# Performance work log

Measured on AMD Instinct MI355X. Metric: run time of the kernel, lower is better.

Reference implementation:

```python
import jax, jax.numpy as jnp
import numpy as np

N, IN, HID, OUT, HD = 512, 256, 256, 256, 64  # n_agents, in_dim, hid_dim, out_dim, head_dim (out_dim // n_heads)


def _mlp2(x, w1, b1, w2, b2):
    return jax.nn.relu(x @ w1.T + b1) @ w2.T + b2


def setup_inputs():
    key = jax.random.key(0)
    ks = jax.random.split(key, 32)
    p = lambda i, shape: jax.random.normal(ks[i], shape, dtype=jnp.float32) * 0.05
    V = jax.random.normal(ks[0], (N, IN), dtype=jnp.float32)
    adj = jax.random.randint(ks[1], (N, N), 0, 2, dtype=jnp.int32)
    adj = adj.at[jnp.arange(N), jnp.arange(N)].set(1)  # self-loops so no softmax row is all -inf
    prev_hidden = jax.random.normal(ks[2], (N, HID), dtype=jnp.float32)
    return {
        "V": V, "adj": adj, "prev_hidden": prev_hidden,
        "W1": p(3, (HID, IN)), "sa0": p(4, (HID,)), "sa1": p(5, (HID,)),
        "ce_w1": p(6, (HID, 2 * IN)), "ce_b1": p(7, (HID,)), "ce_w2": p(8, (HD, HID)), "ce_b2": p(9, (HD,)),
        "ca0": p(10, (HD,)), "ca1": p(11, (HD,)),
        "te_w1": p(12, (HID, IN + HID)), "te_b1": p(13, (HID,)), "te_w2": p(14, (HD, HID)), "te_b2": p(15, (HD,)),
        "ta0": p(16, (HD,)), "ta1": p(17, (HD,)),
        "pe_w1": p(18, (HID, 3 * IN)), "pe_b1": p(19, (HID,)), "pe_w2": p(20, (HD, HID)), "pe_b2": p(21, (HD,)),
        "pa0": p(22, (HD,)), "pa1": p(23, (HD,)),
        "W2": p(24, (OUT, HID + 2 * HD + 1)), "op_w": p(25, (OUT, OUT)), "op_b": p(26, (OUT,)),
        "ln_g": jnp.ones((OUT,), jnp.float32), "ln_b": jnp.zeros((OUT,), jnp.float32),
    }


def _forward(V, adj, prev_hidden, W1, sa0, sa1, ce_w1, ce_b1, ce_w2, ce_b2, ca0, ca1,
             te_w1, te_b1, te_w2, te_b2, ta0, ta1, pe_w1, pe_b1, pe_w2, pe_b2, pa0, pa1,
             W2, op_w, op_b, ln_g, ln_b):
    neg = -jnp.inf
    # --- branch 1: standard GAT attention ---
    Wh1 = V @ W1.T                                             # (N, HID)
    s1 = (Wh1 @ sa0)[:, None] + (Wh1 @ sa1)[None, :]           # (N, N)
    s1 = jnp.where(adj == 0, neg, s1)
    H1 = jax.nn.softmax(s1, axis=1) @ Wh1                      # (N, HID)
    # --- branch 2: causal, all ordered pairs i != j ---
    wA, wB = ce_w1[:, :IN], ce_w1[:, IN:]
    h = jax.nn.relu((V @ wA.T)[:, None, :] + (V @ wB.T)[None, :, :] + ce_b1)  # (N, N, HID)
    f = h @ ce_w2.T + ce_b2                                    # (N, N, HD)
    s2 = jnp.where(jnp.eye(N, dtype=bool), neg, f @ (ca0 + ca1))
    a2 = jax.nn.softmax(s2.reshape(-1)).reshape(N, N)          # softmax over all off-diagonal pairs
    H2 = jnp.broadcast_to(jnp.einsum('ij,ijd->d', a2, f), (N, HD))
    # --- branch 3: temporal; (N,1) scores broadcast against (N,N) causal mask ---
    tf = _mlp2(jnp.concatenate([V, prev_hidden], -1), te_w1, te_b1, te_w2, te_b2)  # (N, HD)
    ts = tf @ (ta0 + ta1)                                      # (N,)
    cmask = jnp.triu(jnp.ones((N, N), dtype=bool), 1)
    s3 = jnp.where(cmask, neg, jnp.broadcast_to(ts[:, None], (N, N)))
    H3 = jax.nn.softmax(s3, axis=1) @ tf                       # (N, HD) == prefix means of tf
    # --- branch 4: cooperative; first two neighbors in index order (zeros if < 2) ---
    pos = jnp.where(adj == 1, jnp.arange(N)[None, :], N)
    srt = jnp.sort(pos, axis=1)
    i0, i1 = srt[:, 0], srt[:, 1]
    valid = (i1 < N)[:, None]
    n0 = jnp.where(valid, V[jnp.clip(i0, 0, N - 1)], 0.0)
    n1 = jnp.where(valid, V[jnp.clip(i1, 0, N - 1)], 0.0)
    cf = _mlp2(jnp.concatenate([V, n0, n1], -1), pe_w1, pe_b1, pe_w2, pe_b2)  # (N, HD)
    # torch: softmax over dim of size 1 -> all ones, alpha^T @ cf == column sums -> (HD,)
    # then unsqueezed to (HD,1) and zero-padded to (N,1) since HD < N  (faithful to source bug)
    H4v = cf.sum(axis=0)
    H4 = jnp.concatenate([H4v, jnp.zeros((N - HD,), V.dtype)])[:, None]       # (N, 1)
    # --- combine ---
    Hc = jnp.concatenate([H1, H2, H3, H4], axis=-1) @ W2.T     # (N, OUT)
    out = Hc @ op_w.T + op_b
    mu = out.mean(-1, keepdims=True)
    var = ((out - mu) ** 2).mean(-1, keepdims=True)
    y = (out - mu) / jnp.sqrt(var + 1e-5) * ln_g + ln_b        # LayerNorm, eps=1e-5
    return jax.nn.elu(y)                                       # dropout is identity in eval


def reference(V, adj, prev_hidden, W1, sa0, sa1, ce_w1, ce_b1, ce_w2, ce_b2, ca0, ca1,
              te_w1, te_b1, te_w2, te_b2, ta0, ta1, pe_w1, pe_b1, pe_w2, pe_b2, pa0, pa1,
              W2, op_w, op_b, ln_g, ln_b):
    return _forward(V, adj, prev_hidden, W1, sa0, sa1, ce_w1, ce_b1, ce_w2, ce_b2, ca0, ca1,
                    te_w1, te_b1, te_w2, te_b2, ta0, ta1, pe_w1, pe_b1, pe_w2, pe_b2, pa0, pa1,
                    W2, op_w, op_b, ln_g, ln_b)
```

## Files before the change

kernel.cpp:

```cpp
#include <hip/hip_runtime.h>

typedef unsigned short u16;

constexpr int kN   = 512;
constexpr int kIN  = 256;
constexpr int kHID = 256;
constexpr int kHD  = 64;
constexpr int kOUT = 256;

__device__ __forceinline__ float us2f(u16 u){
  union { unsigned int i; float f; } c; c.i = ((unsigned int)u) << 16; return c.f;
}
__device__ __forceinline__ u16 f2us(float f){
  union { float f; unsigned int i; } c; c.f = f;
  unsigned int r = c.i + 0x7fff + ((c.i >> 16) & 1);
  return (u16)(r >> 16);
}

__global__ void k_probe(const unsigned int* __restrict__ V, int* __restrict__ flag){
  __shared__ int cnt;
  if (threadIdx.x == 0) cnt = 0;
  __syncthreads();
  int c = 0;
  for (int k = threadIdx.x; k < 4096; k += 256){
    float x = us2f((u16)(V[k] & 0xffffu));
    float ax = fabsf(x);
    if (!(ax <= 32.0f)) c++;
  }
  atomicAdd(&cnt, c);
  __syncthreads();
  if (threadIdx.x == 0) *flag = (cnt > 64) ? 1 : 0;
}

struct ConvArgs { const void* src[23]; float* dst[23]; int n[23]; };

__global__ void k_convert_all(ConvArgs a, const int* __restrict__ flag){
  bool f32 = (*flag != 0);
  int stride = gridDim.x * blockDim.x;
  int t = blockIdx.x * blockDim.x + threadIdx.x;
  for (int s = 0; s < 23; ++s){
    int n4 = a.n[s] >> 2;
    float4* d = (float4*)a.dst[s];
    if (f32){
      const float4* sf = (const float4*)a.src[s];
      for (int i = t; i < n4; i += stride) d[i] = sf[i];
    } else {
      const ushort4* sb = (const ushort4*)a.src[s];
      for (int i = t; i < n4; i += stride){
        ushort4 u = sb[i];
        d[i] = make_float4(us2f(u.x), us2f(u.y), us2f(u.z), us2f(u.w));
      }
    }
  }
}

__device__ __forceinline__ float blk_red(float v, float* tmp, bool isMax){
  int lane = threadIdx.x & 63, wv = threadIdx.x >> 6;
  #pragma unroll
  for (int o = 32; o > 0; o >>= 1){
    float t = __shfl_down(v, o, 64);
    v = isMax ? fmaxf(v, t) : (v + t);
  }
  __syncthreads();
  if (lane == 0) tmp[wv] = v;
  __syncthreads();
  float r = tmp[0];
  for (int i = 1; i < 4; ++i) r = isMax ? fmaxf(r, tmp[i]) : (r + tmp[i]);
  return r;
}

struct WSP {
  const int* adj; const int* flag; void* out;
  float *Vf,*prevf,*W1f,*sa1f,*cw1f,*cb1f,*cw2f,*cb2f,*ca0f,*ca1f;
  float *tw1f,*tb1f,*tw2f,*tb2f,*pw1f,*pb1f,*pw2f,*pb2f;
  float *W2f,*opwf,*opbf,*lngf,*lnbf;
  float *Wh1,*e1v,*minv,*invzv,*H1p,*H1,*Am,*Bm,*uvec,*beta;
  float *s2,*maxp,*zp,*MZ,*gsum,*c2v;
  float *htp0,*htp1,*hpp0,*hpp1,*hpp2,*hidden_t,*hidden_p;
  float *tfp0,*tfp1,*tfp2,*tfp3,*cfp0,*cfp1,*cfp2,*cfp3;
  float *tfm,*cfm,*H3,*H4v,*Xp;
};

struct GSeg2 { const float* X; const float* W; float* C; int ldx, ldw, ldc, K; };
struct GArgs2 { GSeg2 s[8]; };

__device__ __forceinline__ void gemm_body(const GSeg2 sg, int tm, int tn, int tid,
                                          float* xsB, float* wsB)
{
  const int i0 = tm << 7;
  const int n0 = tn << 6;
  const int xrow = tid >> 3;
  const int xk   = (tid & 7) << 2;
  const int rg = (tid >> 4) << 3;
  const int cg = (tid & 15) << 2;

  const float* Xb = sg.X + (size_t)i0 * sg.ldx;
  const float* Wb = sg.W + (size_t)n0 * sg.ldw;

  float4 xr[4], wr[2];
  auto loadT = [&](int kt){
    #pragma unroll
    for (int i2 = 0; i2 < 4; ++i2)
      xr[i2] = *(const float4*)(Xb + (size_t)(xrow + 32*i2) * sg.ldx + kt + xk);
    #pragma unroll
    for (int i2 = 0; i2 < 2; ++i2)
      wr[i2] = *(const float4*)(Wb + (size_t)(xrow + 32*i2) * sg.ldw + kt + xk);
  };
  auto writeT = [&](int bu){
    float* xs = xsB + bu*4224;
    #pragma unroll
    for (int i2 = 0; i2 < 4; ++i2){
      xs[(xk+0)*132 + xrow+32*i2] = xr[i2].x;
      xs[(xk+1)*132 + xrow+32*i2] = xr[i2].y;
      xs[(xk+2)*132 + xrow+32*i2] = xr[i2].z;
      xs[(xk+3)*132 + xrow+32*i2] = xr[i2].w;
    }
    float* ws2 = wsB + bu*2176;
    #pragma unroll
    for (int i2 = 0; i2 < 2; ++i2){
      ws2[(xk+0)*68 + xrow+32*i2] = wr[i2].x;
      ws2[(xk+1)*68 + xrow+32*i2] = wr[i2].y;
      ws2[(xk+2)*68 + xrow+32*i2] = wr[i2].z;
      ws2[(xk+3)*68 + xrow+32*i2] = wr[i2].w;
    }
  };

  loadT(0); writeT(0); __syncthreads();

  float acc[8][4] = {};
  const int nkt = sg.K >> 5;
  for (int t = 0; t < nkt; ++t){
    if (t + 1 < nkt) loadT((t + 1) << 5);
    const float* xs  = xsB + (t & 1)*4224;
    const float* ws2 = wsB + (t & 1)*2176;
    #pragma unroll
    for (int kk = 0; kk < 32; ++kk){
      const float4 a0 = *(const float4*)&xs[kk*132 + rg];
      const float4 a1 = *(const float4*)&xs[kk*132 + rg + 4];
      const float4 bv = *(const float4*)&ws2[kk*68 + cg];
      acc[0][0]+=a0.x*bv.x; acc[0][1]+=a0.x*bv.y; acc[0][2]+=a0.x*bv.z; acc[0][3]+=a0.x*bv.w;
      acc[1][0]+=a0.y*bv.x; acc[1][1]+=a0.y*bv.y; acc[1][2]+=a0.y*bv.z; acc[1][3]+=a0.y*bv.w;
      acc[2][0]+=a0.z*bv.x; acc[2][1]+=a0.z*bv.y; acc[2][2]+=a0.z*bv.z; acc[2][3]+=a0.z*bv.w;
      acc[3][0]+=a0.w*bv.x; acc[3][1]+=a0.w*bv.y; acc[3][2]+=a0.w*bv.z; acc[3][3]+=a0.w*bv.w;
      acc[4][0]+=a1.x*bv.x; acc[4][1]+=a1.x*bv.y; acc[4][2]+=a1.x*bv.z; acc[4][3]+=a1.x*bv.w;
      acc[5][0]+=a1.y*bv.x; acc[5][1]+=a1.y*bv.y; acc[5][2]+=a1.y*bv.z; acc[5][3]+=a1.y*bv.w;
      acc[6][0]+=a1.z*bv.x; acc[6][1]+=a1.z*bv.y; acc[6][2]+=a1.z*bv.z; acc[6][3]+=a1.z*bv.w;
      acc[7][0]+=a1.w*bv.x; acc[7][1]+=a1.w*bv.y; acc[7][2]+=a1.w*bv.z; acc[7][3]+=a1.w*bv.w;
    }
    if (t + 1 < nkt) writeT((t + 1) & 1);
    __syncthreads();
  }

  #pragma unroll
  for (int ri = 0; ri < 8; ++ri)
    *(float4*)(sg.C + (size_t)(i0 + rg + ri) * sg.ldc + (n0 + cg)) =
      make_float4(acc[ri][0], acc[ri][1], acc[ri][2], acc[ri][3]);
}

__global__ __launch_bounds__(256) void k_gemmA(GArgs2 ga)
{
  __shared__ __align__(16) float xsB[2*4224];
  __shared__ __align__(16) float wsB[2*2176];
  const GSeg2 sg = ga.s[blockIdx.y];
  gemm_body(sg, blockIdx.x & 3, blockIdx.x >> 2, threadIdx.x, xsB, wsB);
}

__global__ __launch_bounds__(256) void k_packsel(const int* __restrict__ adj,
                                                 const float* __restrict__ Vf,
                                                 float* __restrict__ Xp)
{
  __shared__ unsigned long long msk[8];
  __shared__ int sj[2];
  int i = blockIdx.x, tid = threadIdx.x;
  int w = tid >> 6, lane = tid & 63;
  unsigned long long m0 = __ballot(adj[(size_t)i*kN + tid] != 0);
  unsigned long long m1 = __ballot(adj[(size_t)i*kN + 256 + tid] != 0);
  if (lane == 0){ msk[w] = m0; msk[4 + w] = m1; }
  __syncthreads();
  if (tid == 0){
    int j0 = -1, j1 = -1;
    for (int c = 0; c < 8 && j1 < 0; ++c){
      unsigned long long m = msk[c];
      while (m && j1 < 0){
        int b = __builtin_ctzll(m);
        int j = c*64 + b;
        if (j0 < 0) j0 = j; else j1 = j;
        m &= m - 1;
      }
    }
    if (j1 < 0) j0 = -1;
    sj[0] = j0; sj[1] = j1;
  }
  __syncthreads();
  int j0 = sj[0], j1 = sj[1];
  Xp[(size_t)i*768 + tid]       = Vf[(size_t)i*kIN + tid];
  Xp[(size_t)i*768 + 256 + tid] = (j0 >= 0) ? Vf[(size_t)j0*kIN + tid] : 0.f;
  Xp[(size_t)i*768 + 512 + tid] = (j1 >= 0) ? Vf[(size_t)j1*kIN + tid] : 0.f;
}

__global__ __launch_bounds__(256) void k_stage2(WSP w)
{
  __shared__ float sm[64];
  int b = blockIdx.x, tid = threadIdx.x;
  if (b < 128){
    int f = b*256 + tid;
    int c4 = f & 63;
    {
      float4 a = ((const float4*)w.htp0)[f], bb = ((const float4*)w.htp1)[f];
      float4 bi = ((const float4*)w.tb1f)[c4];
      ((float4*)w.hidden_t)[f] = make_float4(
        fmaxf(a.x+bb.x+bi.x,0.f), fmaxf(a.y+bb.y+bi.y,0.f),
        fmaxf(a.z+bb.z+bi.z,0.f), fmaxf(a.w+bb.w+bi.w,0.f));
    }
    {
      float4 a = ((const float4*)w.hpp0)[f], bb = ((const float4*)w.hpp1)[f];
      float4 c = ((const float4*)w.hpp2)[f];
      float4 bi = ((const float4*)w.pb1f)[c4];
      ((float4*)w.hidden_p)[f] = make_float4(
        fmaxf(a.x+bb.x+c.x+bi.x,0.f), fmaxf(a.y+bb.y+c.y+bi.y,0.f),
        fmaxf(a.z+bb.z+c.z+bi.z,0.f), fmaxf(a.w+bb.w+c.w+bi.w,0.f));
    }
  } else if (b < 256){
    int r = (b-128)*4 + (tid >> 6), lane = tid & 63;
    float a = 0.f;
    for (int k = lane; k < kHID; k += 64) a += w.Wh1[(size_t)r*kHID + k] * w.sa1f[k];
    #pragma unroll
    for (int o = 32; o > 0; o >>= 1) a += __shfl_down(a, o, 64);
    if (lane == 0) w.e1v[r] = a;
  } else {
    if (tid < 64){ sm[tid] = w.ca0f[tid] + w.ca1f[tid]; w.H4v[tid] = 0.f; }
    __syncthreads();
    float a = 0.f;
    for (int d = 0; d < kHD; ++d) a += w.cw2f[(size_t)d*kHID + tid] * sm[d];
    w.uvec[tid] = a;
    if (tid == 0){
      float bsum = 0.f;
      for (int d = 0; d < kHD; ++d) bsum += w.cb2f[d] * sm[d];
      *w.beta = bsum;
    }
  }
}

__global__ __launch_bounds__(256) void k_stage3(WSP w, GArgs2 gb)
{
  __shared__ __align__(16) char smem[51200];
  int b = blockIdx.x, tid = threadIdx.x;
  if (b < 32){
    const GSeg2 sg = gb.s[b >> 2];
    gemm_body(sg, b & 3, 0, tid, (float*)smem, (float*)(smem + 33792));
  } else if (b < 544){
    float* red = (float*)smem;
    int i = b - 32;
    int m0 = w.adj[(size_t)i*kN + tid];
    int m1 = w.adj[(size_t)i*kN + tid + 256];
    float ea = w.e1v[tid], eb = w.e1v[tid+256];
    float v0 = m0 ? ea : -1e30f;
    float v1 = m1 ? eb : -1e30f;
    float m = blk_red(fmaxf(v0, v1), red, true);
    float z = blk_red((m0 ? expf(ea-m) : 0.f) + (m1 ? expf(eb-m) : 0.f), red, false);
    if (tid == 0){ w.minv[i] = m; w.invzv[i] = 1.0f / z; }
  } else {
    float* aib = (float*)smem;
    float* uu  = (float*)(smem + 4096);
    int q = b - 544;
    int i0 = (q & 127) * 4, j0 = (q >> 7) * 64;
    int wv = tid >> 6, lane = tid & 63;
    uu[tid] = w.uvec[tid];
    float b1v = w.cb1f[tid];
    #pragma unroll
    for (int r = 0; r < 4; ++r) aib[r*256 + tid] = w.Am[(size_t)(i0+r)*kHID + tid] + b1v;
    __syncthreads();
    int i = i0 + wv, j = j0 + lane;
    const float4* bp = (const float4*)(w.Bm + (size_t)j*kHID);
    float acc = *w.beta;
    #pragma unroll 8
    for (int k4 = 0; k4 < kHID/4; ++k4){
      float4 bv = bp[k4];
      float4 a4 = *(const float4*)&aib[wv*256 + k4*4];
      float4 u4 = *(const float4*)&uu[k4*4];
      acc += fmaxf(a4.x+bv.x,0.f)*u4.x + fmaxf(a4.y+bv.y,0.f)*u4.y
           + fmaxf(a4.z+bv.z,0.f)*u4.z + fmaxf(a4.w+bv.w,0.f)*u4.w;
    }
    if (j == i) acc = -1e30f;
    w.s2[(size_t)i*kN + j] = acc;
    float m = acc;
    #pragma unroll
    for (int o = 32; o > 0; o >>= 1) m = fmaxf(m, __shfl_down(m, o, 64));
    m = __shfl(m, 0, 64);
    float e = expf(acc - m);
    #pragma unroll
    for (int o = 32; o > 0; o >>= 1) e += __shfl_down(e, o, 64);
    if (lane == 0){
      int pb = q*4 + wv;
      w.maxp[pb] = m; w.zp[pb] = e;
    }
  }
}

__global__ __launch_bounds__(256) void k_stage4(WSP w)
{
  __shared__ __align__(16) char smem[4096];
  int b = blockIdx.x, tid = threadIdx.x;
  if (b < 32){
    int f = b*256 + tid;
    int c4 = f & 15;
    {
      float4 a = ((const float4*)w.tfp0)[f], bb = ((const float4*)w.tfp1)[f];
      float4 c = ((const float4*)w.tfp2)[f], d = ((const float4*)w.tfp3)[f];
      float4 bi = ((const float4*)w.tb2f)[c4];
      ((float4*)w.tfm)[f] = make_float4(a.x+bb.x+c.x+d.x+bi.x, a.y+bb.y+c.y+d.y+bi.y,
                                        a.z+bb.z+c.z+d.z+bi.z, a.w+bb.w+c.w+d.w+bi.w);
    }
    float4 cc;
    {
      float4 a = ((const float4*)w.cfp0)[f], bb = ((const float4*)w.cfp1)[f];
      float4 c = ((const float4*)w.cfp2)[f], d = ((const float4*)w.cfp3)[f];
      float4 bi = ((const float4*)w.pb2f)[c4];
      cc = make_float4(a.x+bb.x+c.x+d.x+bi.x, a.y+bb.y+c.y+d.y+bi.y,
                       a.z+bb.z+c.z+d.z+bi.z, a.w+bb.w+c.w+d.w+bi.w);
      ((float4*)w.cfm)[f] = cc;
    }
    float4* red4 = (float4*)smem;
    red4[tid] = cc;
    __syncthreads();
    #pragma unroll
    for (int st = 128; st >= 16; st >>= 1){
      if (tid < st){
        float4 x = red4[tid], y = red4[tid + st];
        red4[tid] = make_float4(x.x+y.x, x.y+y.y, x.z+y.z, x.w+y.w);
      }
      __syncthreads();
    }
    if (tid < 16){
      float4 v = red4[tid];
      atomicAdd(&w.H4v[tid*4+0], v.x);
      atomicAdd(&w.H4v[tid*4+1], v.y);
      atomicAdd(&w.H4v[tid*4+2], v.z);
      atomicAdd(&w.H4v[tid*4+3], v.w);
    }
  } else if (b < 1056){
    float* wt = (float*)smem;
    int q = b - 32;
    int i0 = (q & 127) * 4, jt = q >> 7, j0 = jt * 64;
    {
      int r = tid >> 6, jj = tid & 63;
      int j = j0 + jj;
      wt[r*64 + jj] = w.adj[(size_t)(i0+r)*kN + j]
                    ? expf(w.e1v[j] - w.minv[i0+r]) * w.invzv[i0+r] : 0.f;
    }
    __syncthreads();
    float a0=0,a1=0,a2=0,a3=0;
    #pragma unroll 4
    for (int jj = 0; jj < 64; ++jj){
      float wh = w.Wh1[(size_t)(j0+jj)*kHID + tid];
      a0 += wt[jj]*wh; a1 += wt[64+jj]*wh; a2 += wt[128+jj]*wh; a3 += wt[192+jj]*wh;
    }
    size_t base = ((size_t)jt*kN + i0)*kHID + tid;
    w.H1p[base]          = a0;
    w.H1p[base + kHID]   = a1;
    w.H1p[base + 2*kHID] = a2;
    w.H1p[base + 3*kHID] = a3;
  } else {
    float* red = (float*)smem;
    float m = -1e30f;
    #pragma unroll
    for (int r = 0; r < 16; ++r) m = fmaxf(m, w.maxp[tid + 256*r]);
    m = blk_red(m, red, true);
    float z = 0.f;
    #pragma unroll
    for (int r = 0; r < 16; ++r) z += w.zp[tid + 256*r] * expf(w.maxp[tid + 256*r] - m);
    z = blk_red(z, red, false);
    if (tid == 0){ w.MZ[0] = m; w.MZ[1] = z; }
    w.gsum[tid] = 0.f;
  }
}

__global__ __launch_bounds__(256) void k_stage5(WSP w)
{
  __shared__ __align__(16) char smem[1536];
  int b = blockIdx.x, tid = threadIdx.x;
  if (b < 1024){
    float* wt = (float*)smem;
    int i0 = (b & 31) * 16, j0 = (b >> 5) * 16;
    float M = w.MZ[0], invZ = 1.0f / w.MZ[1];
    {
      int r = tid >> 4, c = tid & 15;
      wt[r*16 + c] = expf(w.s2[(size_t)(i0+r)*kN + (j0+c)] - M) * invZ;
    }
    float b1v = w.cb1f[tid];
    float aib[16];
    #pragma unroll
    for (int r = 0; r < 16; ++r) aib[r] = w.Am[(size_t)(i0+r)*kHID + tid] + b1v;
    __syncthreads();
    float acc = 0.f;
    for (int j = 0; j < 16; ++j){
      float bj = w.Bm[(size_t)(j0+j)*kHID + tid];
      #pragma unroll
      for (int r = 0; r < 16; ++r)
        acc += wt[r*16 + j] * fmaxf(aib[r] + bj, 0.f);
    }
    atomicAdd(&w.gsum[tid], acc);
  } else if (b < 1536){
    int i = b - 1024;
    float s = 0.f;
    #pragma unroll
    for (int jt = 0; jt < 8; ++jt)
      s += w.H1p[((size_t)jt*kN + i)*kHID + tid];
    w.H1[(size_t)i*kHID + tid] = s;
  } else {
    int d = b - 1536;
    int lane = tid & 63, wv = tid >> 6;
    float v0 = w.tfm[(size_t)(2*tid)*kHD + d];
    float v1 = w.tfm[(size_t)(2*tid+1)*kHD + d];
    float s = v0 + v1;
    float x = s;
    #pragma unroll
    for (int off = 1; off < 64; off <<= 1){
      float y = __shfl_up(x, off, 64);
      if (lane >= off) x += y;
    }
    float* wsum = (float*)smem;
    if (lane == 63) wsum[wv] = x;
    __syncthreads();
    float base = 0.f;
    for (int k = 0; k < wv; ++k) base += wsum[k];
    float excl = base + x - s;
    w.H3[(size_t)(2*tid)*kHD + d]   = (excl + v0) / (float)(2*tid + 1);
    w.H3[(size_t)(2*tid+1)*kHD + d] = (excl + s)  / (float)(2*tid + 2);
  }
}

__global__ void k_h2c(WSP w)
{
  __shared__ float gs[kHID];
  __shared__ float part[kHD][4];
  __shared__ float h2s[kHD];
  int tid = threadIdx.x;
  gs[tid] = w.gsum[tid];
  __syncthreads();
  int d = tid >> 2, q = tid & 3;
  float a = 0.f;
  for (int kk = 0; kk < 64; ++kk){
    int k = q*64 + kk;
    a += gs[k] * w.cw2f[(size_t)d*kHID + k];
  }
  part[d][q] = a;
  __syncthreads();
  if (tid < kHD)
    h2s[tid] = w.cb2f[tid] + part[tid][0] + part[tid][1] + part[tid][2] + part[tid][3];
  __syncthreads();
  float c = 0.f;
  const float* wr = w.W2f + (size_t)tid*385 + 256;
  for (int dd = 0; dd < kHD; ++dd) c += h2s[dd] * wr[dd];
  w.c2v[tid] = c;
}

__global__ __launch_bounds__(256) void k_outfin(WSP w)
{
  __shared__ float h1s[kHID];
  __shared__ float h3s[kHD];
  __shared__ float row[kOUT];
  __shared__ float red[8];
  __shared__ float h4sh;
  int i = blockIdx.x, o = threadIdx.x;
  h1s[o] = w.H1[(size_t)i*kHID + o];
  if (o < kHD) h3s[o] = w.H3[(size_t)i*kHD + o];
  if (o == 0)  h4sh = (i < kHD) ? w.H4v[i] : 0.f;
  __syncthreads();
  const float* wr = w.W2f + (size_t)o * 385;
  float acc = w.c2v[o];
  for (int k = 0; k < kHID; ++k) acc += h1s[k] * wr[k];
  for (int dd = 0; dd < kHD; ++dd) acc += h3s[dd] * wr[320+dd];
  acc += h4sh * wr[384];
  row[o] = acc;
  __syncthreads();
  const float4* opr = (const float4*)(w.opwf + (size_t)o * kOUT);
  float a2 = w.opbf[o];
  for (int kb = 0; kb < 64; ++kb){
    float4 qv = opr[kb];
    a2 += row[kb*4]*qv.x + row[kb*4+1]*qv.y + row[kb*4+2]*qv.z + row[kb*4+3]*qv.w;
  }
  float mu = blk_red(a2, red, false) * (1.0f/kOUT);
  float dv = a2 - mu;
  float var = blk_red(dv*dv, red, false) * (1.0f/kOUT);
  float y = dv * rsqrtf(var + 1e-5f) * w.lngf[o] + w.lnbf[o];
  y = (y > 0.f) ? y : expm1f(y);
  if (*w.flag) ((float*)w.out)[(size_t)i*kOUT + o] = y;
  else         ((u16*)w.out)[(size_t)i*kOUT + o]   = f2us(y);
}

extern "C" void kernel_launch(void* const* d_in, const int* in_sizes, int n_in,
                              void* d_out, int out_size, void* d_ws, size_t ws_size,
                              hipStream_t stream)
{
  const void* V     = d_in[0];
  const int*  adj   = (const int*)d_in[1];
  const void* prev  = d_in[2];
  const void* W1    = d_in[3];
  const void* sa1   = d_in[5];
  const void* ce_w1 = d_in[6];
  const void* ce_b1 = d_in[7];
  const void* ce_w2 = d_in[8];
  const void* ce_b2 = d_in[9];
  const void* ca0   = d_in[10];
  const void* ca1   = d_in[11];
  const void* te_w1 = d_in[12];
  const void* te_b1 = d_in[13];
  const void* te_w2 = d_in[14];
  const void* te_b2 = d_in[15];
  const void* pe_w1 = d_in[18];
  const void* pe_b1 = d_in[19];
  const void* pe_w2 = d_in[20];
  const void* pe_b2 = d_in[21];
  const void* W2    = d_in[24];
  const void* op_w  = d_in[25];
  const void* op_b  = d_in[26];
  const void* ln_g  = d_in[27];
  const void* ln_b  = d_in[28];

  float* ws  = (float*)d_ws;
  int*  flag = (int*)ws;
  float* p   = ws + 16;
  float* Vf   = p; p += 131072;
  float* prevf= p; p += 131072;
  float* W1f  = p; p += 65536;
  float* sa1f = p; p += 256;
  float* cw1f = p; p += 131072;
  float* cb1f = p; p += 256;
  float* cw2f = p; p += 16384;
  float* cb2f = p; p += 64;
  float* ca0f = p; p += 64;
  float* ca1f = p; p += 64;
  float* tw1f = p; p += 131072;
  float* tb1f = p; p += 256;
  float* tw2f = p; p += 16384;
  float* tb2f = p; p += 64;
  float* pw1f = p; p += 196608;
  float* pb1f = p; p += 256;
  float* pw2f = p; p += 16384;
  float* pb2f = p; p += 64;
  float* W2f  = p; p += 98560;
  float* opwf = p; p += 65536;
  float* opbf = p; p += 256;
  float* lngf = p; p += 256;
  float* lnbf = p; p += 256;
  float* Wh1      = p; p += 131072;
  float* e1v      = p; p += 512;
  float* minv     = p; p += 512;
  float* invzv    = p; p += 512;
  float* H1p      = p; p += 1048576;
  float* H1       = p; p += 131072;
  float* Am       = p; p += 131072;
  float* Bm       = p; p += 131072;
  float* uvec     = p; p += 256;
  float* beta     = p; p += 16;
  float* s2       = p; p += 262144;
  float* maxp     = p; p += 4096;
  float* zpart    = p; p += 4096;
  float* MZ       = p; p += 16;
  float* gsum     = p; p += 256;
  float* c2v      = p; p += 256;
  float* htp0     = p; p += 131072;
  float* htp1     = p; p += 131072;
  float* hpp0     = p; p += 131072;
  float* hpp1     = p; p += 131072;
  float* hpp2     = p; p += 131072;
  float* hidden_t = p; p += 131072;
  float* hidden_p = p; p += 131072;
  float* tfp0     = p; p += 32768;
  float* tfp1     = p; p += 32768;
  float* tfp2     = p; p += 32768;
  float* tfp3     = p; p += 32768;
  float* cfp0     = p; p += 32768;
  float* cfp1     = p; p += 32768;
  float* cfp2     = p; p += 32768;
  float* cfp3     = p; p += 32768;
  float* tfm      = p; p += 32768;
  float* cfm      = p; p += 32768;
  float* H3       = p; p += 32768;
  float* H4v      = p; p += 64;
  float* Xp       = p; p += 393216;

  k_probe<<<1, 256, 0, stream>>>((const unsigned int*)V, flag);
  ConvArgs ca;
  const void* srcs[23] = {V, prev, W1, sa1, ce_w1, ce_b1, ce_w2, ce_b2, ca0, ca1,
                          te_w1, te_b1, te_w2, te_b2, pe_w1, pe_b1, pe_w2, pe_b2,
                          W2, op_w, op_b, ln_g, ln_b};
  float* dsts[23] = {Vf, prevf, W1f, sa1f, cw1f, cb1f, cw2f, cb2f, ca0f, ca1f,
                     tw1f, tb1f, tw2f, tb2f, pw1f, pb1f, pw2f, pb2f,
                     W2f, opwf, opbf, lngf, lnbf};
  int ns[23] = {131072, 131072, 65536, 256, 131072, 256, 16384, 64, 64, 64,
                131072, 256, 16384, 64, 196608, 256, 16384, 64,
                98560, 65536, 256, 256, 256};
  for (int s = 0; s < 23; ++s){ ca.src[s] = srcs[s]; ca.dst[s] = dsts[s]; ca.n[s] = ns[s]; }
  k_convert_all<<<256, 256, 0, stream>>>(ca, flag);

  WSP w;
  w.adj = adj; w.flag = flag; w.out = d_out;
  w.Vf=Vf; w.prevf=prevf; w.W1f=W1f; w.sa1f=sa1f; w.cw1f=cw1f; w.cb1f=cb1f;
  w.cw2f=cw2f; w.cb2f=cb2f; w.ca0f=ca0f; w.ca1f=ca1f;
  w.tw1f=tw1f; w.tb1f=tb1f; w.tw2f=tw2f; w.tb2f=tb2f;
  w.pw1f=pw1f; w.pb1f=pb1f; w.pw2f=pw2f; w.pb2f=pb2f;
  w.W2f=W2f; w.opwf=opwf; w.opbf=opbf; w.lngf=lngf; w.lnbf=lnbf;
  w.Wh1=Wh1; w.e1v=e1v; w.minv=minv; w.invzv=invzv; w.H1p=H1p; w.H1=H1;
  w.Am=Am; w.Bm=Bm; w.uvec=uvec; w.beta=beta;
  w.s2=s2; w.maxp=maxp; w.zp=zpart; w.MZ=MZ; w.gsum=gsum; w.c2v=c2v;
  w.htp0=htp0; w.htp1=htp1; w.hpp0=hpp0; w.hpp1=hpp1; w.hpp2=hpp2;
  w.hidden_t=hidden_t; w.hidden_p=hidden_p;
  w.tfp0=tfp0; w.tfp1=tfp1; w.tfp2=tfp2; w.tfp3=tfp3;
  w.cfp0=cfp0; w.cfp1=cfp1; w.cfp2=cfp2; w.cfp3=cfp3;
  w.tfm=tfm; w.cfm=cfm; w.H3=H3; w.H4v=H4v; w.Xp=Xp;

  k_packsel<<<kN, 256, 0, stream>>>(adj, Vf, Xp);

  {
    GArgs2 g{};
    g.s[0] = {Vf,       W1f,        Wh1,  256, 256, 256, 256};
    g.s[1] = {Vf,       cw1f,       Am,   256, 512, 256, 256};
    g.s[2] = {Vf,       cw1f + 256, Bm,   256, 512, 256, 256};
    g.s[3] = {Vf,       tw1f,       htp0, 256, 512, 256, 256};
    g.s[4] = {prevf,    tw1f + 256, htp1, 256, 512, 256, 256};
    g.s[5] = {Xp,       pw1f,       hpp0, 768, 768, 256, 256};
    g.s[6] = {Xp + 256, pw1f + 256, hpp1, 768, 768, 256, 256};
    g.s[7] = {Xp + 512, pw1f + 512, hpp2, 768, 768, 256, 256};
    k_gemmA<<<dim3(16, 8), 256, 0, stream>>>(g);
  }

  k_stage2<<<257, 256, 0, stream>>>(w);

  {
    GArgs2 gb{};
    for (int k = 0; k < 4; ++k){
      gb.s[k]   = {hidden_t + 64*k, tw2f + 64*k,
                   (k==0?tfp0:k==1?tfp1:k==2?tfp2:tfp3), 256, 256, 64, 64};
      gb.s[4+k] = {hidden_p + 64*k, pw2f + 64*k,
                   (k==0?cfp0:k==1?cfp1:k==2?cfp2:cfp3), 256, 256, 64, 64};
    }
    k_stage3<<<1568, 256, 0, stream>>>(w, gb);
  }

  k_stage4<<<1057, 256, 0, stream>>>(w);

  k_stage5<<<1600, 256, 0, stream>>>(w);

  k_h2c<<<1, 256, 0, stream>>>(w);

  k_outfin<<<kN, 256, 0, stream>>>(w);
}
```

Baseline: 277.6 us.

## Fuse probe/convert/packsel, shrink GEMM tiles, and fold small kernels into stages

```diff
diff --git a/kernel.cpp b/kernel.cpp
--- a/kernel.cpp
+++ b/kernel.cpp
@@ -17,40 +17,79 @@
   return (u16)(r >> 16);
 }
 
-__global__ void k_probe(const unsigned int* __restrict__ V, int* __restrict__ flag){
+__device__ bool probe_is_f32(const unsigned int* __restrict__ V){
   __shared__ int cnt;
   if (threadIdx.x == 0) cnt = 0;
   __syncthreads();
   int c = 0;
   for (int k = threadIdx.x; k < 4096; k += 256){
     float x = us2f((u16)(V[k] & 0xffffu));
-    float ax = fabsf(x);
-    if (!(ax <= 32.0f)) c++;
+    if (!(fabsf(x) <= 32.0f)) c++;
   }
   atomicAdd(&cnt, c);
   __syncthreads();
-  if (threadIdx.x == 0) *flag = (cnt > 64) ? 1 : 0;
+  return cnt > 64;
 }
 
 struct ConvArgs { const void* src[23]; float* dst[23]; int n[23]; };
 
-__global__ void k_convert_all(ConvArgs a, const int* __restrict__ flag){
-  bool f32 = (*flag != 0);
-  int stride = gridDim.x * blockDim.x;
-  int t = blockIdx.x * blockDim.x + threadIdx.x;
-  for (int s = 0; s < 23; ++s){
-    int n4 = a.n[s] >> 2;
-    float4* d = (float4*)a.dst[s];
-    if (f32){
-      const float4* sf = (const float4*)a.src[s];
-      for (int i = t; i < n4; i += stride) d[i] = sf[i];
-    } else {
-      const ushort4* sb = (const ushort4*)a.src[s];
-      for (int i = t; i < n4; i += stride){
-        ushort4 u = sb[i];
-        d[i] = make_float4(us2f(u.x), us2f(u.y), us2f(u.z), us2f(u.w));
+__global__ __launch_bounds__(256) void k_conv(ConvArgs a, const unsigned int* __restrict__ Vraw,
+                                              const int* __restrict__ adj, int* __restrict__ flag,
+                                              float* __restrict__ Xp)
+{
+  int b = blockIdx.x, tid = threadIdx.x;
+  bool f32 = probe_is_f32(Vraw);
+  if (b < 256){
+    if (b == 0 && tid == 0) *flag = f32 ? 1 : 0;
+    int t = b*256 + tid;
+    const int stride = 65536;
+    for (int s = 0; s < 23; ++s){
+      int n4 = a.n[s] >> 2;
+      float4* d = (float4*)a.dst[s];
+      if (f32){
+        const float4* sf = (const float4*)a.src[s];
+        for (int i = t; i < n4; i += stride) d[i] = sf[i];
+      } else {
+        const ushort4* sb = (const ushort4*)a.src[s];
+        for (int i = t; i < n4; i += stride){
+          ushort4 u = sb[i];
+          d[i] = make_float4(us2f(u.x), us2f(u.y), us2f(u.z), us2f(u.w));
+        }
       }
     }
+  } else {
+    __shared__ unsigned long long msk[8];
+    __shared__ int sj[2];
+    int i = b - 256;
+    int w = tid >> 6, lane = tid & 63;
+    unsigned long long m0 = __ballot(adj[(size_t)i*kN + tid] != 0);
+    unsigned long long m1 = __ballot(adj[(size_t)i*kN + 256 + tid] != 0);
+    if (lane == 0){ msk[w] = m0; msk[4 + w] = m1; }
+    __syncthreads();
+    if (tid == 0){
+      int j0 = -1, j1 = -1;
+      for (int c = 0; c < 8 && j1 < 0; ++c){
+        unsigned long long m = msk[c];
+        while (m && j1 < 0){
+          int bb = __builtin_ctzll(m);
+          int j = c*64 + bb;
+          if (j0 < 0) j0 = j; else j1 = j;
+          m &= m - 1;
+        }
+      }
+      if (j1 < 0) j0 = -1;
+      sj[0] = j0; sj[1] = j1;
+    }
+    __syncthreads();
+    int j0 = sj[0], j1 = sj[1];
+    const float* Vf = (const float*)Vraw;
+    const u16*  Vb = (const u16*)Vraw;
+    auto rdV = [&](int r, int k)->float{
+      return f32 ? Vf[(size_t)r*kIN + k] : us2f(Vb[(size_t)r*kIN + k]);
+    };
+    Xp[(size_t)i*768 + tid]       = rdV(i, tid);
+    Xp[(size_t)i*768 + 256 + tid] = (j0 >= 0) ? rdV(j0, tid) : 0.f;
+    Xp[(size_t)i*768 + 512 + tid] = (j1 >= 0) ? rdV(j1, tid) : 0.f;
   }
 }
 
@@ -74,133 +113,77 @@
   float *Vf,*prevf,*W1f,*sa1f,*cw1f,*cb1f,*cw2f,*cb2f,*ca0f,*ca1f;
   float *tw1f,*tb1f,*tw2f,*tb2f,*pw1f,*pb1f,*pw2f,*pb2f;
   float *W2f,*opwf,*opbf,*lngf,*lnbf;
+  float *tw2t,*pw2t,*W2t;
   float *Wh1,*e1v,*minv,*invzv,*H1p,*H1,*Am,*Bm,*uvec,*beta;
-  float *s2,*maxp,*zp,*MZ,*gsum,*c2v;
+  float *s2,*maxp,*zp,*MZ,*gsum;
   float *htp0,*htp1,*hpp0,*hpp1,*hpp2,*hidden_t,*hidden_p;
-  float *tfp0,*tfp1,*tfp2,*tfp3,*cfp0,*cfp1,*cfp2,*cfp3;
   float *tfm,*cfm,*H3,*H4v,*Xp;
 };
 
 struct GSeg2 { const float* X; const float* W; float* C; int ldx, ldw, ldc, K; };
 struct GArgs2 { GSeg2 s[8]; };
 
-__device__ __forceinline__ void gemm_body(const GSeg2 sg, int tm, int tn, int tid,
-                                          float* xsB, float* wsB)
-{
-  const int i0 = tm << 7;
+__global__ __launch_bounds__(256) void k_gemmA(GArgs2 ga)
+{
+  __shared__ __align__(16) float Xs[2][32][36];
+  __shared__ __align__(16) float Ws[2][32][68];
+  const GSeg2 sg = ga.s[blockIdx.y];
+  const int tm = blockIdx.x & 15;
+  const int tn = blockIdx.x >> 4;
+  const int i0 = tm << 5;
   const int n0 = tn << 6;
+  const int tid = threadIdx.x;
+
   const int xrow = tid >> 3;
   const int xk   = (tid & 7) << 2;
-  const int rg = (tid >> 4) << 3;
+  const int rg = (tid >> 4) << 1;
   const int cg = (tid & 15) << 2;
 
   const float* Xb = sg.X + (size_t)i0 * sg.ldx;
   const float* Wb = sg.W + (size_t)n0 * sg.ldw;
 
-  float4 xr[4], wr[2];
+  float4 xr, wr0, wr1;
   auto loadT = [&](int kt){
-    #pragma unroll
-    for (int i2 = 0; i2 < 4; ++i2)
-      xr[i2] = *(const float4*)(Xb + (size_t)(xrow + 32*i2) * sg.ldx + kt + xk);
-    #pragma unroll
-    for (int i2 = 0; i2 < 2; ++i2)
-      wr[i2] = *(const float4*)(Wb + (size_t)(xrow + 32*i2) * sg.ldw + kt + xk);
+    xr  = *(const float4*)(Xb + (size_t)xrow * sg.ldx + kt + xk);
+    wr0 = *(const float4*)(Wb + (size_t)xrow * sg.ldw + kt + xk);
+    wr1 = *(const float4*)(Wb + (size_t)(xrow+32) * sg.ldw + kt + xk);
   };
   auto writeT = [&](int bu){
-    float* xs = xsB + bu*4224;
-    #pragma unroll
-    for (int i2 = 0; i2 < 4; ++i2){
-      xs[(xk+0)*132 + xrow+32*i2] = xr[i2].x;
-      xs[(xk+1)*132 + xrow+32*i2] = xr[i2].y;
-      xs[(xk+2)*132 + xrow+32*i2] = xr[i2].z;
-      xs[(xk+3)*132 + xrow+32*i2] = xr[i2].w;
-    }
-    float* ws2 = wsB + bu*2176;
-    #pragma unroll
-    for (int i2 = 0; i2 < 2; ++i2){
-      ws2[(xk+0)*68 + xrow+32*i2] = wr[i2].x;
-      ws2[(xk+1)*68 + xrow+32*i2] = wr[i2].y;
-      ws2[(xk+2)*68 + xrow+32*i2] = wr[i2].z;
-      ws2[(xk+3)*68 + xrow+32*i2] = wr[i2].w;
-    }
+    Xs[bu][xk+0][xrow] = xr.x;  Xs[bu][xk+1][xrow] = xr.y;
+    Xs[bu][xk+2][xrow] = xr.z;  Xs[bu][xk+3][xrow] = xr.w;
+    Ws[bu][xk+0][xrow]    = wr0.x; Ws[bu][xk+1][xrow]    = wr0.y;
+    Ws[bu][xk+2][xrow]    = wr0.z; Ws[bu][xk+3][xrow]    = wr0.w;
+    Ws[bu][xk+0][xrow+32] = wr1.x; Ws[bu][xk+1][xrow+32] = wr1.y;
+    Ws[bu][xk+2][xrow+32] = wr1.z; Ws[bu][xk+3][xrow+32] = wr1.w;
   };
 
   loadT(0); writeT(0); __syncthreads();
 
-  float acc[8][4] = {};
+  float acc[2][4] = {};
   const int nkt = sg.K >> 5;
   for (int t = 0; t < nkt; ++t){
     if (t + 1 < nkt) loadT((t + 1) << 5);
-    const float* xs  = xsB + (t & 1)*4224;
-    const float* ws2 = wsB + (t & 1)*2176;
+    const int bu = t & 1;
     #pragma unroll
     for (int kk = 0; kk < 32; ++kk){
-      const float4 a0 = *(const float4*)&xs[kk*132 + rg];
-      const float4 a1 = *(const float4*)&xs[kk*132 + rg + 4];
-      const float4 bv = *(const float4*)&ws2[kk*68 + cg];
-      acc[0][0]+=a0.x*bv.x; acc[0][1]+=a0.x*bv.y; acc[0][2]+=a0.x*bv.z; acc[0][3]+=a0.x*bv.w;
-      acc[1][0]+=a0.y*bv.x; acc[1][1]+=a0.y*bv.y; acc[1][2]+=a0.y*bv.z; acc[1][3]+=a0.y*bv.w;
-      acc[2][0]+=a0.z*bv.x; acc[2][1]+=a0.z*bv.y; acc[2][2]+=a0.z*bv.z; acc[2][3]+=a0.z*bv.w;
-      acc[3][0]+=a0.w*bv.x; acc[3][1]+=a0.w*bv.y; acc[3][2]+=a0.w*bv.z; acc[3][3]+=a0.w*bv.w;
-      acc[4][0]+=a1.x*bv.x; acc[4][1]+=a1.x*bv.y; acc[4][2]+=a1.x*bv.z; acc[4][3]+=a1.x*bv.w;
-      acc[5][0]+=a1.y*bv.x; acc[5][1]+=a1.y*bv.y; acc[5][2]+=a1.y*bv.z; acc[5][3]+=a1.y*bv.w;
-      acc[6][0]+=a1.z*bv.x; acc[6][1]+=a1.z*bv.y; acc[6][2]+=a1.z*bv.z; acc[6][3]+=a1.z*bv.w;
-      acc[7][0]+=a1.w*bv.x; acc[7][1]+=a1.w*bv.y; acc[7][2]+=a1.w*bv.z; acc[7][3]+=a1.w*bv.w;
+      const float2 av = *(const float2*)&Xs[bu][kk][rg];
+      const float4 bv = *(const float4*)&Ws[bu][kk][cg];
+      acc[0][0]+=av.x*bv.x; acc[0][1]+=av.x*bv.y; acc[0][2]+=av.x*bv.z; acc[0][3]+=av.x*bv.w;
+      acc[1][0]+=av.y*bv.x; acc[1][1]+=av.y*bv.y; acc[1][2]+=av.y*bv.z; acc[1][3]+=av.y*bv.w;
     }
     if (t + 1 < nkt) writeT((t + 1) & 1);
     __syncthreads();
   }
 
   #pragma unroll
-  for (int ri = 0; ri < 8; ++ri)
+  for (int ri = 0; ri < 2; ++ri)
     *(float4*)(sg.C + (size_t)(i0 + rg + ri) * sg.ldc + (n0 + cg)) =
       make_float4(acc[ri][0], acc[ri][1], acc[ri][2], acc[ri][3]);
 }
 
-__global__ __launch_bounds__(256) void k_gemmA(GArgs2 ga)
-{
-  __shared__ __align__(16) float xsB[2*4224];
-  __shared__ __align__(16) float wsB[2*2176];
-  const GSeg2 sg = ga.s[blockIdx.y];
-  gemm_body(sg, blockIdx.x & 3, blockIdx.x >> 2, threadIdx.x, xsB, wsB);
-}
-
-__global__ __launch_bounds__(256) void k_packsel(const int* __restrict__ adj,
-                                                 const float* __restrict__ Vf,
-                                                 float* __restrict__ Xp)
-{
-  __shared__ unsigned long long msk[8];
-  __shared__ int sj[2];
-  int i = blockIdx.x, tid = threadIdx.x;
-  int w = tid >> 6, lane = tid & 63;
-  unsigned long long m0 = __ballot(adj[(size_t)i*kN + tid] != 0);
-  unsigned long long m1 = __ballot(adj[(size_t)i*kN + 256 + tid] != 0);
-  if (lane == 0){ msk[w] = m0; msk[4 + w] = m1; }
-  __syncthreads();
-  if (tid == 0){
-    int j0 = -1, j1 = -1;
-    for (int c = 0; c < 8 && j1 < 0; ++c){
-      unsigned long long m = msk[c];
-      while (m && j1 < 0){
-        int b = __builtin_ctzll(m);
-        int j = c*64 + b;
-        if (j0 < 0) j0 = j; else j1 = j;
-        m &= m - 1;
-      }
-    }
-    if (j1 < 0) j0 = -1;
-    sj[0] = j0; sj[1] = j1;
-  }
-  __syncthreads();
-  int j0 = sj[0], j1 = sj[1];
-  Xp[(size_t)i*768 + tid]       = Vf[(size_t)i*kIN + tid];
-  Xp[(size_t)i*768 + 256 + tid] = (j0 >= 0) ? Vf[(size_t)j0*kIN + tid] : 0.f;
-  Xp[(size_t)i*768 + 512 + tid] = (j1 >= 0) ? Vf[(size_t)j1*kIN + tid] : 0.f;
-}
-
 __global__ __launch_bounds__(256) void k_stage2(WSP w)
 {
-  __shared__ float sm[64];
+  __shared__ float st[64*65];
   int b = blockIdx.x, tid = threadIdx.x;
   if (b < 128){
     int f = b*256 + tid;
@@ -227,30 +210,84 @@
     #pragma unroll
     for (int o = 32; o > 0; o >>= 1) a += __shfl_down(a, o, 64);
     if (lane == 0) w.e1v[r] = a;
-  } else {
-    if (tid < 64){ sm[tid] = w.ca0f[tid] + w.ca1f[tid]; w.H4v[tid] = 0.f; }
+  } else if (b == 256){
+    if (tid < 64){ st[tid] = w.ca0f[tid] + w.ca1f[tid]; w.H4v[tid] = 0.f; }
     __syncthreads();
     float a = 0.f;
-    for (int d = 0; d < kHD; ++d) a += w.cw2f[(size_t)d*kHID + tid] * sm[d];
+    for (int d = 0; d < kHD; ++d) a += w.cw2f[(size_t)d*kHID + tid] * st[d];
     w.uvec[tid] = a;
     if (tid == 0){
       float bsum = 0.f;
-      for (int d = 0; d < kHD; ++d) bsum += w.cb2f[d] * sm[d];
+      for (int d = 0; d < kHD; ++d) bsum += w.cb2f[d] * st[d];
       *w.beta = bsum;
     }
-  }
-}
-
-__global__ __launch_bounds__(256) void k_stage3(WSP w, GArgs2 gb)
-{
-  __shared__ __align__(16) char smem[51200];
+  } else if (b < 259){
+    const float* src = (b == 257) ? w.tw2f : w.pw2f;
+    float* dst = (b == 257) ? w.tw2t : w.pw2t;
+    for (int ch = 0; ch < 4; ++ch){
+      __syncthreads();
+      #pragma unroll
+      for (int e = 0; e < 16; ++e){
+        int lin = e*256 + tid;
+        int r = lin >> 6, c = lin & 63;
+        st[r*65 + c] = src[(size_t)r*256 + ch*64 + c];
+      }
+      __syncthreads();
+      #pragma unroll
+      for (int e = 0; e < 16; ++e){
+        int lin = e*256 + tid;
+        int kc = lin >> 6, dd = lin & 63;
+        dst[(size_t)(ch*64 + kc)*64 + dd] = st[dd*65 + kc];
+      }
+    }
+  } else {
+    int c0 = (b - 259) * 4;
+    for (int cc = 0; cc < 4; ++cc){
+      int c = c0 + cc;
+      if (c < 385) w.W2t[(size_t)c*256 + tid] = w.W2f[(size_t)tid*385 + c];
+    }
+  }
+}
+
+__global__ __launch_bounds__(256) void k_stage3(WSP w)
+{
+  __shared__ __align__(16) float smem3[4*256 + 256];
   int b = blockIdx.x, tid = threadIdx.x;
-  if (b < 32){
-    const GSeg2 sg = gb.s[b >> 2];
-    gemm_body(sg, b & 3, 0, tid, (float*)smem, (float*)(smem + 33792));
-  } else if (b < 544){
-    float* red = (float*)smem;
-    int i = b - 32;
+  if (b < 64){
+    int m = b >> 5, grp = b & 31;
+    const float* X  = m ? w.hidden_p : w.hidden_t;
+    const float* Wt = m ? w.pw2t : w.tw2t;
+    const float* bi = m ? w.pb2f : w.tb2f;
+    float* C = m ? w.cfm : w.tfm;
+    int i0 = grp*16 + (tid >> 6)*4;
+    int d = tid & 63;
+    const float* x0 = X + (size_t)i0*256;
+    const float* x1 = x0 + 256;
+    const float* x2 = x0 + 512;
+    const float* x3 = x0 + 768;
+    float a0=0.f, a1=0.f, a2=0.f, a3=0.f;
+    for (int k = 0; k < 256; k += 4){
+      float w0 = Wt[(size_t)(k+0)*64 + d];
+      float w1 = Wt[(size_t)(k+1)*64 + d];
+      float w2 = Wt[(size_t)(k+2)*64 + d];
+      float w3 = Wt[(size_t)(k+3)*64 + d];
+      float4 f0 = *(const float4*)(x0 + k);
+      float4 f1 = *(const float4*)(x1 + k);
+      float4 f2 = *(const float4*)(x2 + k);
+      float4 f3 = *(const float4*)(x3 + k);
+      a0 += f0.x*w0 + f0.y*w1 + f0.z*w2 + f0.w*w3;
+      a1 += f1.x*w0 + f1.y*w1 + f1.z*w2 + f1.w*w3;
+      a2 += f2.x*w0 + f2.y*w1 + f2.z*w2 + f2.w*w3;
+      a3 += f3.x*w0 + f3.y*w1 + f3.z*w2 + f3.w*w3;
+    }
+    float bd = bi[d];
+    C[(size_t)(i0+0)*64 + d] = a0 + bd;
+    C[(size_t)(i0+1)*64 + d] = a1 + bd;
+    C[(size_t)(i0+2)*64 + d] = a2 + bd;
+    C[(size_t)(i0+3)*64 + d] = a3 + bd;
+  } else if (b < 576){
+    float* red = smem3;
+    int i = b - 64;
     int m0 = w.adj[(size_t)i*kN + tid];
     int m1 = w.adj[(size_t)i*kN + tid + 256];
     float ea = w.e1v[tid], eb = w.e1v[tid+256];
@@ -260,9 +297,9 @@
     float z = blk_red((m0 ? expf(ea-m) : 0.f) + (m1 ? expf(eb-m) : 0.f), red, false);
     if (tid == 0){ w.minv[i] = m; w.invzv[i] = 1.0f / z; }
   } else {
-    float* aib = (float*)smem;
-    float* uu  = (float*)(smem + 4096);
-    int q = b - 544;
+    float* aib = smem3;
+    float* uu  = smem3 + 1024;
+    int q = b - 576;
     int i0 = (q & 127) * 4, j0 = (q >> 7) * 64;
     int wv = tid >> 6, lane = tid & 63;
     uu[tid] = w.uvec[tid];
@@ -299,48 +336,21 @@
 
 __global__ __launch_bounds__(256) void k_stage4(WSP w)
 {
-  __shared__ __align__(16) char smem[4096];
+  __shared__ __align__(16) float smem[272];
   int b = blockIdx.x, tid = threadIdx.x;
-  if (b < 32){
-    int f = b*256 + tid;
-    int c4 = f & 15;
-    {
-      float4 a = ((const float4*)w.tfp0)[f], bb = ((const float4*)w.tfp1)[f];
-      float4 c = ((const float4*)w.tfp2)[f], d = ((const float4*)w.tfp3)[f];
-      float4 bi = ((const float4*)w.tb2f)[c4];
-      ((float4*)w.tfm)[f] = make_float4(a.x+bb.x+c.x+d.x+bi.x, a.y+bb.y+c.y+d.y+bi.y,
-                                        a.z+bb.z+c.z+d.z+bi.z, a.w+bb.w+c.w+d.w+bi.w);
-    }
-    float4 cc;
-    {
-      float4 a = ((const float4*)w.cfp0)[f], bb = ((const float4*)w.cfp1)[f];
-      float4 c = ((const float4*)w.cfp2)[f], d = ((const float4*)w.cfp3)[f];
-      float4 bi = ((const float4*)w.pb2f)[c4];
-      cc = make_float4(a.x+bb.x+c.x+d.x+bi.x, a.y+bb.y+c.y+d.y+bi.y,
-                       a.z+bb.z+c.z+d.z+bi.z, a.w+bb.w+c.w+d.w+bi.w);
-      ((float4*)w.cfm)[f] = cc;
-    }
-    float4* red4 = (float4*)smem;
-    red4[tid] = cc;
-    __syncthreads();
-    #pragma unroll
-    for (int st = 128; st >= 16; st >>= 1){
-      if (tid < st){
-        float4 x = red4[tid], y = red4[tid + st];
-        red4[tid] = make_float4(x.x+y.x, x.y+y.y, x.z+y.z, x.w+y.w);
-      }
-      __syncthreads();
-    }
-    if (tid < 16){
-      float4 v = red4[tid];
-      atomicAdd(&w.H4v[tid*4+0], v.x);
-      atomicAdd(&w.H4v[tid*4+1], v.y);
-      atomicAdd(&w.H4v[tid*4+2], v.z);
-      atomicAdd(&w.H4v[tid*4+3], v.w);
-    }
-  } else if (b < 1056){
-    float* wt = (float*)smem;
-    int q = b - 32;
+  if (b < 8){
+    int d = tid & 63, sub = tid >> 6;
+    int r0 = b*64 + sub*16;
+    float s = 0.f;
+    #pragma unroll
+    for (int e = 0; e < 16; ++e) s += w.cfm[(size_t)(r0+e)*kHD + d];
+    smem[sub*64 + d] = s;
+    __syncthreads();
+    if (tid < 64)
+      atomicAdd(&w.H4v[tid], smem[tid] + smem[64+tid] + smem[128+tid] + smem[192+tid]);
+  } else if (b < 1032){
+    float* wt = smem;
+    int q = b - 8;
     int i0 = (q & 127) * 4, jt = q >> 7, j0 = jt * 64;
     {
       int r = tid >> 6, jj = tid & 63;
@@ -361,7 +371,7 @@
     w.H1p[base + 2*kHID] = a2;
     w.H1p[base + 3*kHID] = a3;
   } else {
-    float* red = (float*)smem;
+    float* red = smem;
     float m = -1e30f;
     #pragma unroll
     for (int r = 0; r < 16; ++r) m = fmaxf(m, w.maxp[tid + 256*r]);
@@ -430,48 +440,42 @@
   }
 }
 
-__global__ void k_h2c(WSP w)
-{
-  __shared__ float gs[kHID];
+__global__ __launch_bounds__(256) void k_outfin(WSP w)
+{
+  __shared__ float h1s[kHID];
+  __shared__ float gssh[kHID];
   __shared__ float part[kHD][4];
   __shared__ float h2s[kHD];
-  int tid = threadIdx.x;
-  gs[tid] = w.gsum[tid];
-  __syncthreads();
-  int d = tid >> 2, q = tid & 3;
-  float a = 0.f;
-  for (int kk = 0; kk < 64; ++kk){
-    int k = q*64 + kk;
-    a += gs[k] * w.cw2f[(size_t)d*kHID + k];
-  }
-  part[d][q] = a;
-  __syncthreads();
-  if (tid < kHD)
-    h2s[tid] = w.cb2f[tid] + part[tid][0] + part[tid][1] + part[tid][2] + part[tid][3];
-  __syncthreads();
-  float c = 0.f;
-  const float* wr = w.W2f + (size_t)tid*385 + 256;
-  for (int dd = 0; dd < kHD; ++dd) c += h2s[dd] * wr[dd];
-  w.c2v[tid] = c;
-}
-
-__global__ __launch_bounds__(256) void k_outfin(WSP w)
-{
-  __shared__ float h1s[kHID];
   __shared__ float h3s[kHD];
   __shared__ float row[kOUT];
-  __shared__ float red[8];
+  __shared__ float red[4];
   __shared__ float h4sh;
   int i = blockIdx.x, o = threadIdx.x;
   h1s[o] = w.H1[(size_t)i*kHID + o];
+  gssh[o] = w.gsum[o];
   if (o < kHD) h3s[o] = w.H3[(size_t)i*kHD + o];
   if (o == 0)  h4sh = (i < kHD) ? w.H4v[i] : 0.f;
   __syncthreads();
-  const float* wr = w.W2f + (size_t)o * 385;
-  float acc = w.c2v[o];
-  for (int k = 0; k < kHID; ++k) acc += h1s[k] * wr[k];
-  for (int dd = 0; dd < kHD; ++dd) acc += h3s[dd] * wr[320+dd];
-  acc += h4sh * wr[384];
+  {
+    int dd = o >> 2, q = o & 3;
+    float a = 0.f;
+    for (int kk = 0; kk < 64; ++kk){
+      int k = q*64 + kk;
+      a += gssh[k] * w.cw2f[(size_t)dd*kHID + k];
+    }
+    part[dd][q] = a;
+  }
+  __syncthreads();
+  if (o < kHD)
+    h2s[o] = w.cb2f[o] + part[o][0] + part[o][1] + part[o][2] + part[o][3];
+  __syncthreads();
+  float acc = 0.f;
+  for (int k = 0; k < kHID; ++k) acc += h1s[k] * w.W2t[(size_t)k*256 + o];
+  for (int dd = 0; dd < kHD; ++dd){
+    acc += h2s[dd] * w.W2t[(size_t)(256+dd)*256 + o];
+    acc += h3s[dd] * w.W2t[(size_t)(320+dd)*256 + o];
+  }
+  acc += h4sh * w.W2t[(size_t)384*256 + o];
   row[o] = acc;
   __syncthreads();
   const float4* opr = (const float4*)(w.opwf + (size_t)o * kOUT);
@@ -544,6 +548,9 @@
   float* opbf = p; p += 256;
   float* lngf = p; p += 256;
   float* lnbf = p; p += 256;
+  float* tw2t = p; p += 16384;
+  float* pw2t = p; p += 16384;
+  float* W2t  = p; p += 98560;
   float* Wh1      = p; p += 131072;
   float* e1v      = p; p += 512;
   float* minv     = p; p += 512;
@@ -559,7 +566,6 @@
   float* zpart    = p; p += 4096;
   float* MZ       = p; p += 16;
   float* gsum     = p; p += 256;
-  float* c2v      = p; p += 256;
   float* htp0     = p; p += 131072;
   float* htp1     = p; p += 131072;
   float* hpp0     = p; p += 131072;
@@ -567,33 +573,11 @@
   float* hpp2     = p; p += 131072;
   float* hidden_t = p; p += 131072;
   float* hidden_p = p; p += 131072;
-  float* tfp0     = p; p += 32768;
-  float* tfp1     = p; p += 32768;
-  float* tfp2     = p; p += 32768;
-  float* tfp3     = p; p += 32768;
-  float* cfp0     = p; p += 32768;
-  float* cfp1     = p; p += 32768;
-  float* cfp2     = p; p += 32768;
-  float* cfp3     = p; p += 32768;
   float* tfm      = p; p += 32768;
   float* cfm      = p; p += 32768;
   float* H3       = p; p += 32768;
   float* H4v      = p; p += 64;
   float* Xp       = p; p += 393216;
-
-  k_probe<<<1, 256, 0, stream>>>((const unsigned int*)V, flag);
-  ConvArgs ca;
-  const void* srcs[23] = {V, prev, W1, sa1, ce_w1, ce_b1, ce_w2, ce_b2, ca0, ca1,
-                          te_w1, te_b1, te_w2, te_b2, pe_w1, pe_b1, pe_w2, pe_b2,
-                          W2, op_w, op_b, ln_g, ln_b};
-  float* dsts[23] = {Vf, prevf, W1f, sa1f, cw1f, cb1f, cw2f, cb2f, ca0f, ca1f,
-                     tw1f, tb1f, tw2f, tb2f, pw1f, pb1f, pw2f, pb2f,
-                     W2f, opwf, opbf, lngf, lnbf};
-  int ns[23] = {131072, 131072, 65536, 256, 131072, 256, 16384, 64, 64, 64,
-                131072, 256, 16384, 64, 196608, 256, 16384, 64,
-                98560, 65536, 256, 256, 256};
-  for (int s = 0; s < 23; ++s){ ca.src[s] = srcs[s]; ca.dst[s] = dsts[s]; ca.n[s] = ns[s]; }
-  k_convert_all<<<256, 256, 0, stream>>>(ca, flag);
 
   WSP w;
   w.adj = adj; w.flag = flag; w.out = d_out;
@@ -602,16 +586,28 @@
   w.tw1f=tw1f; w.tb1f=tb1f; w.tw2f=tw2f; w.tb2f=tb2f;
   w.pw1f=pw1f; w.pb1f=pb1f; w.pw2f=pw2f; w.pb2f=pb2f;
   w.W2f=W2f; w.opwf=opwf; w.opbf=opbf; w.lngf=lngf; w.lnbf=lnbf;
+  w.tw2t=tw2t; w.pw2t=pw2t; w.W2t=W2t;
   w.Wh1=Wh1; w.e1v=e1v; w.minv=minv; w.invzv=invzv; w.H1p=H1p; w.H1=H1;
   w.Am=Am; w.Bm=Bm; w.uvec=uvec; w.beta=beta;
-  w.s2=s2; w.maxp=maxp; w.zp=zpart; w.MZ=MZ; w.gsum=gsum; w.c2v=c2v;
+  w.s2=s2; w.maxp=maxp; w.zp=zpart; w.MZ=MZ; w.gsum=gsum;
   w.htp0=htp0; w.htp1=htp1; w.hpp0=hpp0; w.hpp1=hpp1; w.hpp2=hpp2;
   w.hidden_t=hidden_t; w.hidden_p=hidden_p;
-  w.tfp0=tfp0; w.tfp1=tfp1; w.tfp2=tfp2; w.tfp3=tfp3;
-  w.cfp0=cfp0; w.cfp1=cfp1; w.cfp2=cfp2; w.cfp3=cfp3;
   w.tfm=tfm; w.cfm=cfm; w.H3=H3; w.H4v=H4v; w.Xp=Xp;
 
-  k_packsel<<<kN, 256, 0, stream>>>(adj, Vf, Xp);
+  {
+    ConvArgs ca;
+    const void* srcs[23] = {V, prev, W1, sa1, ce_w1, ce_b1, ce_w2, ce_b2, ca0, ca1,
+                            te_w1, te_b1, te_w2, te_b2, pe_w1, pe_b1, pe_w2, pe_b2,
+                            W2, op_w, op_b, ln_g, ln_b};
+    float* dsts[23] = {Vf, prevf, W1f, sa1f, cw1f, cb1f, cw2f, cb2f, ca0f, ca1f,
+                       tw1f, tb1f, tw2f, tb2f, pw1f, pb1f, pw2f, pb2f,
+                       W2f, opwf, opbf, lngf, lnbf};
+    int ns[23] = {131072, 131072, 65536, 256, 131072, 256, 16384, 64, 64, 64,
+                  131072, 256, 16384, 64, 196608, 256, 16384, 64,
+                  98560, 65536, 256, 256, 256};
+    for (int s = 0; s < 23; ++s){ ca.src[s] = srcs[s]; ca.dst[s] = dsts[s]; ca.n[s] = ns[s]; }
+    k_conv<<<768, 256, 0, stream>>>(ca, (const unsigned int*)V, adj, flag, Xp);
+  }
 
   {
     GArgs2 g{};
@@ -623,27 +619,16 @@
     g.s[5] = {Xp,       pw1f,       hpp0, 768, 768, 256, 256};
     g.s[6] = {Xp + 256, pw1f + 256, hpp1, 768, 768, 256, 256};
     g.s[7] = {Xp + 512, pw1f + 512, hpp2, 768, 768, 256, 256};
-    k_gemmA<<<dim3(16, 8), 256, 0, stream>>>(g);
-  }
-
-  k_stage2<<<257, 256, 0, stream>>>(w);
-
-  {
-    GArgs2 gb{};
-    for (int k = 0; k < 4; ++k){
-      gb.s[k]   = {hidden_t + 64*k, tw2f + 64*k,
-                   (k==0?tfp0:k==1?tfp1:k==2?tfp2:tfp3), 256, 256, 64, 64};
-      gb.s[4+k] = {hidden_p + 64*k, pw2f + 64*k,
-                   (k==0?cfp0:k==1?cfp1:k==2?cfp2:cfp3), 256, 256, 64, 64};
-    }
-    k_stage3<<<1568, 256, 0, stream>>>(w, gb);
-  }
-
-  k_stage4<<<1057, 256, 0, stream>>>(w);
+    k_gemmA<<<dim3(64, 8), 256, 0, stream>>>(g);
+  }
+
+  k_stage2<<<356, 256, 0, stream>>>(w);
+
+  k_stage3<<<1600, 256, 0, stream>>>(w);
+
+  k_stage4<<<1033, 256, 0, stream>>>(w);
 
   k_stage5<<<1600, 256, 0, stream>>>(w);
 
-  k_h2c<<<1, 256, 0, stream>>>(w);
-
   k_outfin<<<kN, 256, 0, stream>>>(w);
 }
```

Result: faster. 271.7 us (-2.1%).
